# Kernel optimization log

Hardware: AMD Instinct MI355X
Metric: run time of the kernel (lower is better)

Reference implementation:

```python
import jax, jax.numpy as jnp
import numpy as np

B, C, H, W = 8, 256, 64, 64
DQK = 16  # int(sqrt(out_channels))


def setup_inputs() -> dict:
    key = jax.random.key(0)
    ks = jax.random.split(key, 8)
    s_in = 1.0 / np.sqrt(C)
    return {
        "x": jax.random.normal(ks[0], (B, C, H, W), dtype=jnp.float32),
        "Wf": jax.random.normal(ks[1], (DQK, C), dtype=jnp.float32) * s_in,
        "bf": jnp.zeros((DQK,), dtype=jnp.float32),
        "Wg": jax.random.normal(ks[2], (DQK, C), dtype=jnp.float32) * s_in,
        "bg": jnp.zeros((DQK,), dtype=jnp.float32),
        "Wh": jax.random.normal(ks[3], (C, C), dtype=jnp.float32) * s_in,
        "bh": jnp.zeros((C,), dtype=jnp.float32),
        # original inits attention_multiplier to 0.0; use small nonzero so output depends on attention path
        "gamma": jnp.float32(0.5),
    }


def reference(x, Wf, bf, Wg, bg, Wh, bh, gamma):
    b, c, h, w = x.shape
    hw = h * w
    # 1x1 convs == per-pixel channel projections
    f = (jnp.einsum('bchw,oc->bohw', x, Wf) + bf[None, :, None, None]).reshape(b, -1, hw)  # [B,DQK,HW]
    g = (jnp.einsum('bchw,oc->bohw', x, Wg) + bg[None, :, None, None]).reshape(b, -1, hw)  # [B,DQK,HW]
    hh = (jnp.einsum('bchw,oc->bohw', x, Wh) + bh[None, :, None, None]).reshape(b, -1, hw)  # [B,C,HW]
    # s[b,n,m] = sum_k g[b,k,n] * f[b,k,m]  -> [B,HW,HW]
    s = jnp.einsum('bkn,bkm->bnm', g, f)
    beta = jax.nn.softmax(s, axis=-1)
    # o = beta @ h^T, then transpose back to channel-first: [B,C,HW]
    o = jnp.einsum('bnm,bcm->bcn', beta, hh)
    return gamma * o.reshape(x.shape) + x
```

## Files before the change

### kernel.cpp

```cpp
#include <hip/hip_runtime.h>
#include <math.h>

#define BATCH 8
#define CH    256
#define HWN   4096
#define DQK   16

typedef __attribute__((ext_vector_type(8))) short short8;
typedef __attribute__((ext_vector_type(4))) float float4v;

__device__ __forceinline__ unsigned short f2bf(float f) {
    union { float f; unsigned int u; } v; v.f = f;
    unsigned int r = v.u + 0x7FFF + ((v.u >> 16) & 1);
    return (unsigned short)(r >> 16);
}
__device__ __forceinline__ unsigned int pack2bf(float lo, float hi) {
    union { float f; unsigned int u; } a, b; a.f = lo; b.f = hi;
    unsigned int ra = (a.u + 0x7FFF + ((a.u >> 16) & 1)) >> 16;
    unsigned int rb = (b.u + 0x7FFF + ((b.u >> 16) & 1)) & 0xFFFF0000u;
    return ra | rb;
}

__global__ __launch_bounds__(256) void wcast_kernel(
    const float* __restrict__ Wf, const float* __restrict__ bf_,
    const float* __restrict__ Wg, const float* __restrict__ bg,
    const float* __restrict__ Wh, const float* __restrict__ bh,
    unsigned short* __restrict__ Wbf, float* __restrict__ bcat)
{
    const int r = blockIdx.x;
    const int t = threadIdx.x;
    const float* src = (r < 16) ? (Wf + r*CH) : (r < 32) ? (Wg + (r-16)*CH) : (Wh + (r-32)*CH);
    Wbf[r*CH + t] = f2bf(src[t]);
    if (t == 0) bcat[r] = (r < 16) ? bf_[r] : (r < 32) ? bg[r-16] : bh[r-32];
}

__global__ __launch_bounds__(256) void xt_kernel(const float* __restrict__ x,
                                                 unsigned short* __restrict__ xt)
{
    const int t  = threadIdx.x;
    const int p0 = blockIdx.x * 64;
    const int c0 = blockIdx.y * 64;
    const int b  = blockIdx.z;
    __shared__ unsigned short tile[64][73];
    const int pc = t & 63;
    const int r0 = (t >> 6) * 16;
    #pragma unroll
    for (int j = 0; j < 16; j++) {
        int c = r0 + j;
        tile[pc][c] = f2bf(x[(size_t)(b*CH + c0 + c)*HWN + p0 + pc]);
    }
    __syncthreads();
    const int pr = t >> 2;
    const int cb = (t & 3) * 16;
    unsigned int outv[8];
    #pragma unroll
    for (int i = 0; i < 8; i++)
        outv[i] = (unsigned int)tile[pr][cb + 2*i] | ((unsigned int)tile[pr][cb + 2*i + 1] << 16);
    unsigned short* dst = &xt[(size_t)(b*HWN + p0 + pr)*CH + c0 + cb];
    *(uint4*)dst       = *(uint4*)&outv[0];
    *(uint4*)(dst + 8) = *(uint4*)&outv[4];
}

__global__ __launch_bounds__(256, 2) void proj_kernel(
    const unsigned short* __restrict__ xt, const unsigned short* __restrict__ Wbf,
    const float* __restrict__ bcat,
    unsigned short* __restrict__ ft, unsigned short* __restrict__ g,
    unsigned short* __restrict__ h2)
{
    const int t    = threadIdx.x;
    const int px0  = blockIdx.x * 64;
    const int b    = blockIdx.y;
    const int lane = t & 63, w = t >> 6, l15 = lane & 15, quad = lane >> 4;
    const int px   = px0 + w*16 + l15;

    float4v acc[18];
    #pragma unroll
    for (int rt = 0; rt < 18; rt++) acc[rt] = (float4v){0.f,0.f,0.f,0.f};

    const unsigned short* xrow = &xt[(size_t)(b*HWN + px)*CH + quad*8];
    const unsigned short* wq   = &Wbf[l15*CH + quad*8];

    #pragma unroll
    for (int ks = 0; ks < 8; ks++) {
        short8 bfrag = *(const short8*)&xrow[ks*32];
        #pragma unroll
        for (int rt = 0; rt < 18; rt++) {
            short8 afrag = *(const short8*)&wq[rt*16*CH + ks*32];
            acc[rt] = __builtin_amdgcn_mfma_f32_16x16x32_bf16(afrag, bfrag, acc[rt], 0, 0, 0);
        }
    }

    const int row_ft = (px & ~31) | (((px & 31) >> 1) + (px & 1) * 16);
    {
        float4 bv = *(const float4*)&bcat[quad*4];
        unsigned int u0 = pack2bf(acc[0][0] + bv.x, acc[0][1] + bv.y);
        unsigned int u1 = pack2bf(acc[0][2] + bv.z, acc[0][3] + bv.w);
        unsigned short* fp = &ft[((size_t)b*HWN + row_ft)*32];
        *(uint2*)&fp[quad*4]      = make_uint2(u0, u1);
        *(uint2*)&fp[16 + quad*4] = make_uint2(0u, 0u);
    }
    {
        float4 bv = *(const float4*)&bcat[16 + quad*4];
        float vb[4] = {bv.x, bv.y, bv.z, bv.w};
        #pragma unroll
        for (int r = 0; r < 4; r++)
            g[(size_t)(b*DQK + quad*4 + r)*HWN + px] = f2bf(acc[1][r] + vb[r]);
    }
    const int mt = px >> 5, mm = px & 31;
    #pragma unroll
    for (int rt = 2; rt < 18; rt++) {
        float4 bv = *(const float4*)&bcat[rt*16 + quad*4];
        float vb[4] = {bv.x, bv.y, bv.z, bv.w};
        #pragma unroll
        for (int r = 0; r < 4; r++) {
            int c = rt*16 + quad*4 + r - 32;
            h2[(((size_t)b*128 + mt)*CH + c)*32 + mm] = f2bf(acc[rt][r] + vb[r]);
        }
    }
}

__global__ __launch_bounds__(256, 2) void attn_kernel(
    const unsigned short* __restrict__ ft, const unsigned short* __restrict__ g,
    const unsigned short* __restrict__ h2, const float* __restrict__ x,
    const float* __restrict__ gamma_p, float* __restrict__ out)
{
    const int t    = threadIdx.x;
    const int b    = blockIdx.x & 7;
    const int q0   = (blockIdx.x >> 3) * 64;
    const int lane = t & 63, w = t >> 6, l15 = lane & 15, quad = lane >> 4;

    __shared__ unsigned int pB[2][4][64][4];

    union { short8 v; unsigned short u[8]; } gfrag, ones;
    #pragma unroll
    for (int j = 0; j < 8; j++) {
        int k = quad*8 + j;
        gfrag.u[j] = (k < DQK) ? g[(size_t)(b*DQK + k)*HWN + q0 + w*16 + l15] : (unsigned short)0;
        ones.u[j]  = (l15 == 0) ? (unsigned short)0x3F80 : (unsigned short)0;
    }

    const unsigned short* ftb = ft + (size_t)b*HWN*32;
    const unsigned short* h2b = h2 + (size_t)b*128*CH*32;

    short8 fr0[2], fr1[2], hr[2][4];
    fr0[0] = *(const short8*)&ftb[(size_t)(l15)*32 + quad*8];
    fr1[0] = *(const short8*)&ftb[(size_t)(16 + l15)*32 + quad*8];
    #pragma unroll
    for (int ct = 0; ct < 4; ct++)
        hr[0][ct] = *(const short8*)&h2b[(size_t)(w*64 + ct*16 + l15)*32 + quad*8];

    float4v acc[4][4], accl[4];
    #pragma unroll
    for (int i = 0; i < 4; i++) {
        accl[i] = (float4v){0.f,0.f,0.f,0.f};
        #pragma unroll
        for (int j = 0; j < 4; j++) acc[i][j] = (float4v){0.f,0.f,0.f,0.f};
    }

    for (int i0 = 0; i0 < 128; i0 += 2) {
        #pragma unroll
        for (int u = 0; u < 2; u++) {
            const int i = i0 + u;
            const int buf = u;
            float4v z = {0.f,0.f,0.f,0.f};
            float4v s0 = __builtin_amdgcn_mfma_f32_16x16x32_bf16(gfrag.v, fr0[buf], z, 0, 0, 0);
            float4v s1 = __builtin_amdgcn_mfma_f32_16x16x32_bf16(gfrag.v, fr1[buf], z, 0, 0, 0);
            unsigned int* pw = &pB[buf][w][quad*16 + (l15 >> 2)][l15 & 3];
            #pragma unroll
            for (int r = 0; r < 4; r++) {
                float pe = __expf(s0[r]);
                float po = __expf(s1[r]);
                pw[16*r] = pack2bf(pe, po);
            }
            __syncthreads();
            const int ni = (i + 1) & 127;
            fr0[buf^1] = *(const short8*)&ftb[((size_t)ni*32 + l15)*32 + quad*8];
            fr1[buf^1] = *(const short8*)&ftb[((size_t)ni*32 + 16 + l15)*32 + quad*8];
            #pragma unroll
            for (int ct = 0; ct < 4; ct++)
                hr[buf^1][ct] = *(const short8*)&h2b[(((size_t)ni*CH) + w*64 + ct*16 + l15)*32 + quad*8];
            short8 bq[4];
            #pragma unroll
            for (int qt = 0; qt < 4; qt++)
                bq[qt] = *(const short8*)&pB[buf][qt][l15*4 + quad][0];
            #pragma unroll
            for (int qt = 0; qt < 4; qt++)
                accl[qt] = __builtin_amdgcn_mfma_f32_16x16x32_bf16(ones.v, bq[qt], accl[qt], 0, 0, 0);
            #pragma unroll
            for (int ct = 0; ct < 4; ct++)
                #pragma unroll
                for (int qt = 0; qt < 4; qt++)
                    acc[ct][qt] = __builtin_amdgcn_mfma_f32_16x16x32_bf16(hr[buf][ct], bq[qt], acc[ct][qt], 0, 0, 0);
        }
    }

    const float gamma = *gamma_p;
    float linv[4];
    #pragma unroll
    for (int qt = 0; qt < 4; qt++) {
        float lv = __shfl(accl[qt][0], lane & 15, 64);
        linv[qt] = 1.f / lv;
    }
    #pragma unroll
    for (int ct = 0; ct < 4; ct++) {
        #pragma unroll
        for (int r = 0; r < 4; r++) {
            int c = w*64 + ct*16 + quad*4 + r;
            size_t base = (size_t)(b*CH + c)*HWN + q0;
            #pragma unroll
            for (int qt = 0; qt < 4; qt++) {
                size_t o = base + qt*16 + l15;
                out[o] = gamma * acc[ct][qt][r] * linv[qt] + x[o];
            }
        }
    }
}

extern "C" void kernel_launch(void* const* d_in, const int* in_sizes, int n_in,
                              void* d_out, int out_size, void* d_ws, size_t ws_size,
                              hipStream_t stream) {
    const float* x     = (const float*)d_in[0];
    const float* Wf    = (const float*)d_in[1];
    const float* bf_   = (const float*)d_in[2];
    const float* Wg    = (const float*)d_in[3];
    const float* bg    = (const float*)d_in[4];
    const float* Wh    = (const float*)d_in[5];
    const float* bh    = (const float*)d_in[6];
    const float* gamma = (const float*)d_in[7];
    float* out = (float*)d_out;

    unsigned short* xt  = (unsigned short*)d_ws;
    unsigned short* ft  = xt  + (size_t)BATCH*HWN*CH;
    unsigned short* g   = ft  + (size_t)BATCH*HWN*32;
    unsigned short* h2  = g   + (size_t)BATCH*DQK*HWN;
    unsigned short* Wbf = h2  + (size_t)BATCH*128*CH*32;
    float*          bcat = (float*)(Wbf + 288*CH);

    wcast_kernel<<<dim3(288), 256, 0, stream>>>(Wf, bf_, Wg, bg, Wh, bh, Wbf, bcat);
    xt_kernel<<<dim3(HWN/64, CH/64, BATCH), 256, 0, stream>>>(x, xt);
    proj_kernel<<<dim3(HWN/64, BATCH), 256, 0, stream>>>(xt, Wbf, bcat, ft, g, h2);
    attn_kernel<<<dim3((HWN/64)*BATCH), 256, 0, stream>>>(ft, g, h2, x, gamma, out);
}
```

Baseline: 240.3 us.

## Re-layout f/h into MFMA-native fragment order and process 64 keys per step

```diff
diff --git a/kernel.cpp b/kernel.cpp
--- a/kernel.cpp
+++ b/kernel.cpp
@@ -19,6 +19,9 @@
     unsigned int ra = (a.u + 0x7FFF + ((a.u >> 16) & 1)) >> 16;
     unsigned int rb = (b.u + 0x7FFF + ((b.u >> 16) & 1)) & 0xFFFF0000u;
     return ra | rb;
+}
+__device__ __forceinline__ int perm_ft(int m) {
+    return (m & ~28) | ((m & 24) >> 1) | ((m & 4) << 2);
 }
 
 __global__ __launch_bounds__(256) void wcast_kernel(
@@ -65,63 +68,61 @@
     const unsigned short* __restrict__ xt, const unsigned short* __restrict__ Wbf,
     const float* __restrict__ bcat,
     unsigned short* __restrict__ ft, unsigned short* __restrict__ g,
-    unsigned short* __restrict__ h2)
+    unsigned short* __restrict__ h3)
 {
     const int t    = threadIdx.x;
     const int px0  = blockIdx.x * 64;
     const int b    = blockIdx.y;
     const int lane = t & 63, w = t >> 6, l15 = lane & 15, quad = lane >> 4;
-    const int px   = px0 + w*16 + l15;
 
     float4v acc[18];
     #pragma unroll
     for (int rt = 0; rt < 18; rt++) acc[rt] = (float4v){0.f,0.f,0.f,0.f};
 
-    const unsigned short* xrow = &xt[(size_t)(b*HWN + px)*CH + quad*8];
-    const unsigned short* wq   = &Wbf[l15*CH + quad*8];
+    const unsigned short* xrow = &xt[((size_t)(b*HWN + px0 + w*16 + l15))*CH + quad*8];
+    const unsigned short* wrow = &Wbf[(size_t)l15*CH + quad*8];
 
     #pragma unroll
     for (int ks = 0; ks < 8; ks++) {
-        short8 bfrag = *(const short8*)&xrow[ks*32];
+        short8 afrag = *(const short8*)&xrow[ks*32];
         #pragma unroll
         for (int rt = 0; rt < 18; rt++) {
-            short8 afrag = *(const short8*)&wq[rt*16*CH + ks*32];
+            short8 bfrag = *(const short8*)&wrow[(size_t)rt*16*CH + ks*32];
             acc[rt] = __builtin_amdgcn_mfma_f32_16x16x32_bf16(afrag, bfrag, acc[rt], 0, 0, 0);
         }
     }
 
-    const int row_ft = (px & ~31) | (((px & 31) >> 1) + (px & 1) * 16);
+    const int pxl = px0 + w*16 + quad*4;
     {
-        float4 bv = *(const float4*)&bcat[quad*4];
-        unsigned int u0 = pack2bf(acc[0][0] + bv.x, acc[0][1] + bv.y);
-        unsigned int u1 = pack2bf(acc[0][2] + bv.z, acc[0][3] + bv.w);
-        unsigned short* fp = &ft[((size_t)b*HWN + row_ft)*32];
-        *(uint2*)&fp[quad*4]      = make_uint2(u0, u1);
-        *(uint2*)&fp[16 + quad*4] = make_uint2(0u, 0u);
+        float bv = bcat[l15];
+        const int s0 = perm_ft(pxl);
+        #pragma unroll
+        for (int r = 0; r < 4; r++) {
+            unsigned short* fp = &ft[((size_t)b*HWN + s0 + r)*32];
+            fp[l15]      = f2bf(acc[0][r] + bv);
+            fp[16 + l15] = 0;
+        }
     }
     {
-        float4 bv = *(const float4*)&bcat[16 + quad*4];
-        float vb[4] = {bv.x, bv.y, bv.z, bv.w};
+        float bv = bcat[16 + l15];
         #pragma unroll
         for (int r = 0; r < 4; r++)
-            g[(size_t)(b*DQK + quad*4 + r)*HWN + px] = f2bf(acc[1][r] + vb[r]);
-    }
-    const int mt = px >> 5, mm = px & 31;
+            g[(size_t)(b*DQK + l15)*HWN + pxl + r] = f2bf(acc[1][r] + bv);
+    }
+    const int mt  = (px0 >> 5) + (w >> 1);
+    const int sub = ((w & 1)*2 + (quad >> 1))*128 + l15*8 + (quad & 1)*4;
     #pragma unroll
     for (int rt = 2; rt < 18; rt++) {
-        float4 bv = *(const float4*)&bcat[rt*16 + quad*4];
-        float vb[4] = {bv.x, bv.y, bv.z, bv.w};
-        #pragma unroll
-        for (int r = 0; r < 4; r++) {
-            int c = rt*16 + quad*4 + r - 32;
-            h2[(((size_t)b*128 + mt)*CH + c)*32 + mm] = f2bf(acc[rt][r] + vb[r]);
-        }
+        float bv = bcat[rt*16 + l15];
+        unsigned int u0 = pack2bf(acc[rt][0] + bv, acc[rt][1] + bv);
+        unsigned int u1 = pack2bf(acc[rt][2] + bv, acc[rt][3] + bv);
+        *(uint2*)&h3[(((size_t)((b*128 + mt)*16 + (rt-2))) << 9) + sub] = make_uint2(u0, u1);
     }
 }
 
 __global__ __launch_bounds__(256, 2) void attn_kernel(
     const unsigned short* __restrict__ ft, const unsigned short* __restrict__ g,
-    const unsigned short* __restrict__ h2, const float* __restrict__ x,
+    const unsigned short* __restrict__ h3, const float* __restrict__ x,
     const float* __restrict__ gamma_p, float* __restrict__ out)
 {
     const int t    = threadIdx.x;
@@ -129,83 +130,94 @@
     const int q0   = (blockIdx.x >> 3) * 64;
     const int lane = t & 63, w = t >> 6, l15 = lane & 15, quad = lane >> 4;
 
-    __shared__ unsigned int pB[2][4][64][4];
-
-    union { short8 v; unsigned short u[8]; } gfrag, ones;
+    __shared__ __align__(16) uint4 pB[2][2][4][64];
+    __shared__ float l_l[64];
+
+    union { short8 v; unsigned short u[8]; } gfrag;
     #pragma unroll
     for (int j = 0; j < 8; j++) {
         int k = quad*8 + j;
         gfrag.u[j] = (k < DQK) ? g[(size_t)(b*DQK + k)*HWN + q0 + w*16 + l15] : (unsigned short)0;
-        ones.u[j]  = (l15 == 0) ? (unsigned short)0x3F80 : (unsigned short)0;
     }
 
     const unsigned short* ftb = ft + (size_t)b*HWN*32;
-    const unsigned short* h2b = h2 + (size_t)b*128*CH*32;
-
-    short8 fr0[2], fr1[2], hr[2][4];
-    fr0[0] = *(const short8*)&ftb[(size_t)(l15)*32 + quad*8];
-    fr1[0] = *(const short8*)&ftb[(size_t)(16 + l15)*32 + quad*8];
-    #pragma unroll
-    for (int ct = 0; ct < 4; ct++)
-        hr[0][ct] = *(const short8*)&h2b[(size_t)(w*64 + ct*16 + l15)*32 + quad*8];
-
-    float4v acc[4][4], accl[4];
-    #pragma unroll
-    for (int i = 0; i < 4; i++) {
-        accl[i] = (float4v){0.f,0.f,0.f,0.f};
+    const unsigned short* h3b = h3 + (((size_t)b*128*16) << 9);
+
+    short8 fr[2][4], hr[2][2][4];
+    float4v acc[4][4];
+    #pragma unroll
+    for (int i = 0; i < 4; i++)
         #pragma unroll
         for (int j = 0; j < 4; j++) acc[i][j] = (float4v){0.f,0.f,0.f,0.f};
-    }
-
-    for (int i0 = 0; i0 < 128; i0 += 2) {
+    float l_acc = 0.f;
+
+    #pragma unroll
+    for (int mt4 = 0; mt4 < 4; mt4++)
+        fr[0][mt4] = *(const short8*)&ftb[(size_t)(mt4*16 + l15)*32 + quad*8];
+    #pragma unroll
+    for (int grp = 0; grp < 2; grp++)
+        #pragma unroll
+        for (int ct = 0; ct < 4; ct++)
+            hr[0][grp][ct] = *(const short8*)&h3b[(((size_t)(grp*16 + w*4 + ct)) << 9) + lane*8];
+
+    for (int i0 = 0; i0 < 64; i0 += 2) {
         #pragma unroll
         for (int u = 0; u < 2; u++) {
             const int i = i0 + u;
-            const int buf = u;
             float4v z = {0.f,0.f,0.f,0.f};
-            float4v s0 = __builtin_amdgcn_mfma_f32_16x16x32_bf16(gfrag.v, fr0[buf], z, 0, 0, 0);
-            float4v s1 = __builtin_amdgcn_mfma_f32_16x16x32_bf16(gfrag.v, fr1[buf], z, 0, 0, 0);
-            unsigned int* pw = &pB[buf][w][quad*16 + (l15 >> 2)][l15 & 3];
-            #pragma unroll
-            for (int r = 0; r < 4; r++) {
-                float pe = __expf(s0[r]);
-                float po = __expf(s1[r]);
-                pw[16*r] = pack2bf(pe, po);
+            float4v s[4];
+            #pragma unroll
+            for (int mt4 = 0; mt4 < 4; mt4++)
+                s[mt4] = __builtin_amdgcn_mfma_f32_16x16x32_bf16(fr[u][mt4], gfrag.v, z, 0, 0, 0);
+            unsigned int P[4][2];
+            #pragma unroll
+            for (int mt4 = 0; mt4 < 4; mt4++) {
+                float e0 = __expf(s[mt4][0]), e1 = __expf(s[mt4][1]);
+                float e2 = __expf(s[mt4][2]), e3 = __expf(s[mt4][3]);
+                l_acc += (e0 + e1) + (e2 + e3);
+                P[mt4][0] = pack2bf(e0, e1);
+                P[mt4][1] = pack2bf(e2, e3);
             }
+            pB[u][0][w][lane] = make_uint4(P[0][0], P[0][1], P[1][0], P[1][1]);
+            pB[u][1][w][lane] = make_uint4(P[2][0], P[2][1], P[3][0], P[3][1]);
             __syncthreads();
-            const int ni = (i + 1) & 127;
-            fr0[buf^1] = *(const short8*)&ftb[((size_t)ni*32 + l15)*32 + quad*8];
-            fr1[buf^1] = *(const short8*)&ftb[((size_t)ni*32 + 16 + l15)*32 + quad*8];
-            #pragma unroll
-            for (int ct = 0; ct < 4; ct++)
-                hr[buf^1][ct] = *(const short8*)&h2b[(((size_t)ni*CH) + w*64 + ct*16 + l15)*32 + quad*8];
-            short8 bq[4];
-            #pragma unroll
-            for (int qt = 0; qt < 4; qt++)
-                bq[qt] = *(const short8*)&pB[buf][qt][l15*4 + quad][0];
-            #pragma unroll
-            for (int qt = 0; qt < 4; qt++)
-                accl[qt] = __builtin_amdgcn_mfma_f32_16x16x32_bf16(ones.v, bq[qt], accl[qt], 0, 0, 0);
-            #pragma unroll
-            for (int ct = 0; ct < 4; ct++)
+            const int ni = (i + 1) & 63;
+            #pragma unroll
+            for (int mt4 = 0; mt4 < 4; mt4++)
+                fr[u^1][mt4] = *(const short8*)&ftb[(size_t)(ni*64 + mt4*16 + l15)*32 + quad*8];
+            #pragma unroll
+            for (int grp = 0; grp < 2; grp++)
                 #pragma unroll
-                for (int qt = 0; qt < 4; qt++)
-                    acc[ct][qt] = __builtin_amdgcn_mfma_f32_16x16x32_bf16(hr[buf][ct], bq[qt], acc[ct][qt], 0, 0, 0);
-        }
-    }
+                for (int ct = 0; ct < 4; ct++)
+                    hr[u^1][grp][ct] = *(const short8*)&h3b[(((size_t)((ni*2 + grp)*16 + w*4 + ct)) << 9) + lane*8];
+            #pragma unroll
+            for (int grp = 0; grp < 2; grp++) {
+                #pragma unroll
+                for (int qt = 0; qt < 4; qt++) {
+                    union { uint4 uu; short8 v; } bq;
+                    bq.uu = pB[u][grp][qt][lane];
+                    #pragma unroll
+                    for (int ct = 0; ct < 4; ct++)
+                        acc[ct][qt] = __builtin_amdgcn_mfma_f32_16x16x32_bf16(hr[u][grp][ct], bq.v, acc[ct][qt], 0, 0, 0);
+                }
+            }
+        }
+    }
+
+    l_acc += __shfl_xor(l_acc, 16, 64);
+    l_acc += __shfl_xor(l_acc, 32, 64);
+    if (quad == 0) l_l[w*16 + l15] = l_acc;
+    __syncthreads();
 
     const float gamma = *gamma_p;
     float linv[4];
     #pragma unroll
-    for (int qt = 0; qt < 4; qt++) {
-        float lv = __shfl(accl[qt][0], lane & 15, 64);
-        linv[qt] = 1.f / lv;
-    }
+    for (int qt = 0; qt < 4; qt++) linv[qt] = 1.f / l_l[qt*16 + l15];
     #pragma unroll
     for (int ct = 0; ct < 4; ct++) {
         #pragma unroll
         for (int r = 0; r < 4; r++) {
-            int c = w*64 + ct*16 + quad*4 + r;
+            int c = (w*4 + ct)*16 + quad*4 + r;
             size_t base = (size_t)(b*CH + c)*HWN + q0;
             #pragma unroll
             for (int qt = 0; qt < 4; qt++) {
@@ -229,15 +241,15 @@
     const float* gamma = (const float*)d_in[7];
     float* out = (float*)d_out;
 
-    unsigned short* xt  = (unsigned short*)d_ws;
-    unsigned short* ft  = xt  + (size_t)BATCH*HWN*CH;
-    unsigned short* g   = ft  + (size_t)BATCH*HWN*32;
-    unsigned short* h2  = g   + (size_t)BATCH*DQK*HWN;
-    unsigned short* Wbf = h2  + (size_t)BATCH*128*CH*32;
+    unsigned short* xt   = (unsigned short*)d_ws;
+    unsigned short* ftp  = xt  + (size_t)BATCH*HWN*CH;
+    unsigned short* g    = ftp + (size_t)BATCH*HWN*32;
+    unsigned short* h3   = g   + (size_t)BATCH*DQK*HWN;
+    unsigned short* Wbf  = h3  + (size_t)BATCH*128*16*512;
     float*          bcat = (float*)(Wbf + 288*CH);
 
     wcast_kernel<<<dim3(288), 256, 0, stream>>>(Wf, bf_, Wg, bg, Wh, bh, Wbf, bcat);
     xt_kernel<<<dim3(HWN/64, CH/64, BATCH), 256, 0, stream>>>(x, xt);
-    proj_kernel<<<dim3(HWN/64, BATCH), 256, 0, stream>>>(xt, Wbf, bcat, ft, g, h2);
-    attn_kernel<<<dim3((HWN/64)*BATCH), 256, 0, stream>>>(ft, g, h2, x, gamma, out);
-}
+    proj_kernel<<<dim3(HWN/64, BATCH), 256, 0, stream>>>(xt, Wbf, bcat, ftp, g, h3);
+    attn_kernel<<<dim3((HWN/64)*BATCH), 256, 0, stream>>>(ftp, g, h3, x, gamma, out);
+}
```

Measured after the change: 222.4 us. -7.4%, faster.
